# Optimization experiments

Hardware: AMD Instinct MI355X
Metric: run time of the kernel (lower is better)

Reference implementation:

```python
import jax, jax.numpy as jnp
import numpy as np

B, D_IN, H = 8192, 4096, 128
E, N, C = 3, 256, 32          # experts, codebook_size, codebook_dim
D1, D2 = 512, 256             # down_units
U1, U2 = 256, 512             # up_units
CW = 0.25                     # commitment_weight


def setup_inputs() -> dict:
    key = jax.random.key(0)
    ks = jax.random.split(key, 16)
    s = 0.02
    f32 = jnp.float32
    inp = {
        'x':   jax.random.normal(ks[0], (B, D_IN), f32),
        # llm_down MLP: 4096 -> 512 -> 256 -> 128 (ReLU on hiddens, linear out)
        'Wd1': jax.random.normal(ks[1], (D_IN, D1), f32) * s, 'bd1': jnp.zeros((D1,), f32),
        'Wd2': jax.random.normal(ks[2], (D1, D2), f32) * s,  'bd2': jnp.zeros((D2,), f32),
        'Wd3': jax.random.normal(ks[3], (D2, H), f32) * s,   'bd3': jnp.zeros((H,), f32),
        # per-expert VQ: project_in 128->32, codebook [256,32], project_out 32->128
        'Win':  jax.random.normal(ks[4], (E, H, C), f32) * s, 'bin_': jnp.zeros((E, C), f32),
        'codebook': jax.random.normal(ks[5], (E, N, C), f32),
        'Wout': jax.random.normal(ks[6], (E, C, H), f32) * s, 'bout': jnp.zeros((E, H), f32),
        # llm_up MLP: 128 -> 256 -> 512 -> 4096
        'Wu1': jax.random.normal(ks[7], (H, U1), f32) * s,   'bu1': jnp.zeros((U1,), f32),
        'Wu2': jax.random.normal(ks[8], (U1, U2), f32) * s,  'bu2': jnp.zeros((U2,), f32),
        'Wu3': jax.random.normal(ks[9], (U2, D_IN), f32) * s, 'bu3': jnp.zeros((D_IN,), f32),
    }
    return inp


def _decorrelation_loss(qemb):
    # qemb: [B, E, H]
    b, e, h = qemb.shape
    cen = qemb - qemb.mean(axis=0, keepdims=True)
    cen = cen.transpose(1, 0, 2).reshape(e, -1)          # [E, B*H]
    cov = (cen @ cen.T) / (b * h - 1)                    # [E, E]
    std = jnp.sqrt(jnp.diag(cov))
    std = jnp.where(std > 1e-8, std, 1.0)
    corr = cov / jnp.outer(std, std)
    c2 = corr ** 2
    return c2.sum() - jnp.diag(c2).sum()


def _vq_experts(latent, Win, bin_, codebook, Wout, bout):
    # latent: [B,H]; all experts share the same (unmasked) latent.
    xe = jnp.einsum('bh,ehc->ebc', latent, Win) + bin_[:, None, :]      # [E,B,C]
    d2 = ((xe ** 2).sum(-1)[..., None]
          - 2.0 * jnp.einsum('ebc,enc->ebn', xe, codebook)
          + (codebook ** 2).sum(-1)[:, None, :])                        # [E,B,N]
    idx = jnp.argmin(d2, axis=-1)                                       # [E,B]
    q = jax.vmap(lambda c, i: c[i])(codebook, idx)                      # [E,B,C] gather
    commit = CW * jnp.mean((jax.lax.stop_gradient(q) - xe) ** 2, axis=(1, 2)).sum()
    quant = xe + jax.lax.stop_gradient(q - xe)                          # straight-through
    qe = jnp.einsum('ebc,ech->ebh', quant, Wout) + bout[:, None, :]     # [E,B,H]
    return qe, idx, commit


def reference(x, Wd1, bd1, Wd2, bd2, Wd3, bd3, Win, bin_, codebook, Wout, bout,
              Wu1, bu1, Wu2, bu2, Wu3, bu3):
    h = jax.nn.relu(x @ Wd1 + bd1)
    h = jax.nn.relu(h @ Wd2 + bd2)
    latent = h @ Wd3 + bd3                                              # [B,128]
    qe, idx, total_commit = _vq_experts(latent, Win, bin_, codebook, Wout, bout)
    qemb = qe.transpose(1, 0, 2)                                        # [B,E,H]
    decorr = _decorrelation_loss(qemb)
    rl = qemb.mean(axis=1)                                              # [B,H]
    u = jax.nn.relu(rl @ Wu1 + bu1)
    u = jax.nn.relu(u @ Wu2 + bu2)
    recon = jnp.clip(u @ Wu3 + bu3, -1.0, 1.0)                          # [B,4096]
    return (recon, idx.T, total_commit, decorr)
```

## Files before the change

### kernel.cpp

```cpp
#include <hip/hip_runtime.h>
#include <hip/hip_bf16.h>

using bf16 = __hip_bfloat16;

typedef __bf16 bf16x8 __attribute__((ext_vector_type(8)));
typedef float  f32x4  __attribute__((ext_vector_type(4)));
typedef unsigned int u32x4 __attribute__((ext_vector_type(4)));
typedef unsigned long long u64;
typedef unsigned short u16;
typedef unsigned int u32;

__device__ __forceinline__ float b2f(bf16 v) { return __bfloat162float(v); }
__device__ __forceinline__ bf16  f2b(float v) { return __float2bfloat16(v); }
__device__ __forceinline__ u16   bits(bf16 v) { return __builtin_bit_cast(u16, v); }

static constexpr size_t SZ_WD1S = 512ull  * 12288 * 2;
static constexpr size_t SZ_WD2S = 256ull  * 1536  * 2;
static constexpr size_t SZ_WFUS = 128ull  * 768   * 2;
static constexpr size_t SZ_WU1T = 256ull  * 128   * 2;
static constexpr size_t SZ_WU2T = 512ull  * 256   * 2;
static constexpr size_t SZ_WU3T = 4096ull * 512   * 2;
static constexpr size_t SZ_H1S  = 8192ull * 1536  * 2;
static constexpr size_t SZ_H2S  = 8192ull * 768   * 2;
static constexpr size_t SZ_XE   = 8192ull * 128   * 4;
static constexpr size_t SZ_QEMB = 3ull * 8192 * 128 * 4;
static constexpr size_t SZ_RL   = 8192ull * 128   * 2;
static constexpr size_t SZ_U1   = 8192ull * 256   * 2;
static constexpr size_t SZ_U2   = 8192ull * 512   * 2;
static constexpr size_t SZ_CNRM = 768ull * 4;
static constexpr size_t SZ_BFUS = 128ull * 4;
static constexpr size_t SZ_PART = 4ull * 8192 * 512 * 4;

static constexpr size_t OFF_WD1S = 0;
static constexpr size_t OFF_WD2S = OFF_WD1S + SZ_WD1S;
static constexpr size_t OFF_WFUS = OFF_WD2S + SZ_WD2S;
static constexpr size_t OFF_WU1T = OFF_WFUS + SZ_WFUS;
static constexpr size_t OFF_WU2T = OFF_WU1T + SZ_WU1T;
static constexpr size_t OFF_WU3T = OFF_WU2T + SZ_WU2T;
static constexpr size_t OFF_H1S  = OFF_WU3T + SZ_WU3T;
static constexpr size_t OFF_H2S  = OFF_H1S  + SZ_H1S;
static constexpr size_t OFF_XE   = OFF_H2S  + SZ_H2S;
static constexpr size_t OFF_QEMB = OFF_XE   + SZ_XE;
static constexpr size_t OFF_RL   = OFF_QEMB + SZ_QEMB;
static constexpr size_t OFF_U1   = OFF_RL   + SZ_RL;
static constexpr size_t OFF_U2   = OFF_U1   + SZ_U1;
static constexpr size_t OFF_CNRM = OFF_U2   + SZ_U2;
static constexpr size_t OFF_BFUS = OFF_CNRM + ((SZ_CNRM + 255) & ~size_t(255));
static constexpr size_t OFF_STAT = OFF_BFUS + ((SZ_BFUS + 255) & ~size_t(255));
static constexpr size_t OFF_PART = OFF_STAT + 2048;

__global__ void wtrans_bf16(const float* __restrict__ in, bf16* __restrict__ out,
                            int K, int N)
{
    __shared__ float tile[32][33];
    const int tx = threadIdx.x, ty = threadIdx.y;
    const int n0 = blockIdx.x * 32, k0 = blockIdx.y * 32;
    #pragma unroll
    for (int i = 0; i < 32; i += 8)
        tile[ty + i][tx] = in[(size_t)(k0 + ty + i) * N + n0 + tx];
    __syncthreads();
    #pragma unroll
    for (int i = 0; i < 32; i += 8)
        out[(size_t)(n0 + ty + i) * K + k0 + tx] = f2b(tile[tx][ty + i]);
}

__global__ void wtrans_split3(const float* __restrict__ in, bf16* __restrict__ out,
                              int K, int N)
{
    __shared__ float tile[32][33];
    const int tx = threadIdx.x, ty = threadIdx.y;
    const int n0 = blockIdx.x * 32, k0 = blockIdx.y * 32;
    #pragma unroll
    for (int i = 0; i < 32; i += 8)
        tile[ty + i][tx] = in[(size_t)(k0 + ty + i) * N + n0 + tx];
    __syncthreads();
    #pragma unroll
    for (int i = 0; i < 32; i += 8) {
        const float v = tile[tx][ty + i];
        const bf16 hi = f2b(v);
        const bf16 lo = f2b(v - b2f(hi));
        bf16* o = out + (size_t)(n0 + ty + i) * 3 * K + 3 * (k0 + tx);
        o[0] = hi; o[1] = lo; o[2] = hi;
    }
}

__global__ void cnorm_kernel(const float* __restrict__ cb, float* __restrict__ cnorm)
{
    const int i = blockIdx.x * blockDim.x + threadIdx.x;
    if (i < 768) {
        float s = 0.f;
        for (int k = 0; k < 32; ++k) { const float v = cb[i * 32 + k]; s += v * v; }
        cnorm[i] = s;
    }
}

__global__ __launch_bounds__(256)
void wfuse_kernel(const float* __restrict__ Wd3, const float* __restrict__ bd3,
                  const float* __restrict__ Win, const float* __restrict__ bin_,
                  bf16* __restrict__ BtS, float* __restrict__ bfuse)
{
    const int n = blockIdx.x;
    const int t = threadIdx.x;
    if (n >= 96) {
        bf16* o = BtS + (size_t)n * 768 + 3 * t;
        o[0] = f2b(0.f); o[1] = f2b(0.f); o[2] = f2b(0.f);
        if (t == 0) bfuse[n] = 0.f;
        return;
    }
    const int e = n >> 5, c = n & 31;
    float s = 0.f;
    for (int h = 0; h < 128; ++h)
        s += Wd3[t * 128 + h] * Win[(size_t)(e * 128 + h) * 32 + c];
    const bf16 hi = f2b(s);
    const bf16 lo = f2b(s - b2f(hi));
    bf16* o = BtS + (size_t)n * 768 + 3 * t;
    o[0] = hi; o[1] = lo; o[2] = hi;
    if (t == 0) {
        float b = bin_[e * 32 + c];
        for (int h = 0; h < 128; ++h)
            b += bd3[h] * Win[(size_t)(e * 128 + h) * 32 + c];
        bfuse[n] = b;
    }
}

__global__ __launch_bounds__(256)
void gemm1_x3(const float* __restrict__ A, const bf16* __restrict__ Bs3,
              float* __restrict__ part)
{
    __shared__ bf16 As[3 * 4096];
    __shared__ bf16 Bs[3 * 4096];
    const int t = threadIdx.x, lane = t & 63, w = t >> 6;
    const int n0 = blockIdx.x * 128;
    const int m0 = blockIdx.y * 128;
    const int kz = blockIdx.z;
    const int wr = w >> 1, wc = w & 1, l15 = lane & 15, quad = lane >> 4;
    const int laneoff = (l15 >> 1) * 64 + (((((l15 & 1) << 2) | quad) ^ ((l15 >> 1) & 7)) << 3);

    f32x4 acc[4][4];
    #pragma unroll
    for (int i = 0; i < 4; ++i)
        #pragma unroll
        for (int j = 0; j < 4; ++j)
            #pragma unroll
            for (int r = 0; r < 4; ++r) acc[i][j][r] = 0.f;

    const int arow = t >> 1, ahalf = t & 1;
    const int ar2 = arow >> 1, arb = (arow & 1) << 2, arx = ar2 & 7;

    int brow[6], bcol[6];
    #pragma unroll
    for (int i = 0; i < 6; ++i) {
        const int p = i * 256 + t;
        const int bkk = p >> 9, br2 = (p >> 3) & 63;
        const int c3 = (p & 7) ^ (br2 & 7);
        brow[i] = 2 * br2 + (c3 >> 2);
        bcol[i] = bkk * 32 + (c3 & 3) * 8;
    }

    const int s0 = kz * 43;
    const int s1 = (kz == 2) ? 128 : (s0 + 43);
    for (int ks = s0; ks < s1; ++ks) {
        const int ko = ks * 32;
        const float* ap = A + (size_t)(m0 + arow) * 4096 + ko + ahalf * 16;
        float f[16];
        *(float4*)(f + 0)  = *(const float4*)(ap + 0);
        *(float4*)(f + 4)  = *(const float4*)(ap + 4);
        *(float4*)(f + 8)  = *(const float4*)(ap + 8);
        *(float4*)(f + 12) = *(const float4*)(ap + 12);
        #pragma unroll
        for (int i = 0; i < 6; ++i) {
            const bf16* gb = Bs3 + (size_t)(n0 + brow[i]) * 12288 + ko * 3 + bcol[i];
            __builtin_amdgcn_global_load_lds(
                (const __attribute__((address_space(1))) void*)gb,
                (__attribute__((address_space(3))) void*)(Bs + (size_t)(i * 256 + t) * 8), 16, 0, 0);
        }
        u32 hi[16], lo[16];
        #pragma unroll
        for (int k = 0; k < 16; ++k) {
            const bf16 hh = f2b(f[k]);
            hi[k] = bits(hh);
            lo[k] = bits(f2b(f[k] - b2f(hh)));
        }
        #pragma unroll
        for (int j = 0; j < 6; ++j) {
            const int cir = ahalf * 6 + j;
            const int kk = cir >> 2, q = cir & 3;
            u32x4 wv;
            #pragma unroll
            for (int i2 = 0; i2 < 4; ++i2) {
                const int e0 = j * 8 + i2 * 2, e1 = e0 + 1;
                const u32 a0 = ((e0 % 3) < 2) ? hi[e0 / 3] : lo[e0 / 3];
                const u32 a1 = ((e1 % 3) < 2) ? hi[e1 / 3] : lo[e1 / 3];
                wv[i2] = a0 | (a1 << 16);
            }
            *(u32x4*)(As + kk * 4096 + ar2 * 64 + (((arb | q) ^ arx) << 3)) = wv;
        }
        __syncthreads();
        #pragma unroll
        for (int kk = 0; kk < 3; ++kk) {
            bf16x8 af[4], bfr[4];
            #pragma unroll
            for (int mi = 0; mi < 4; ++mi)
                af[mi] = *(const bf16x8*)(As + kk * 4096 + wr * 2048 + mi * 512 + laneoff);
            #pragma unroll
            for (int ni = 0; ni < 4; ++ni)
                bfr[ni] = *(const bf16x8*)(Bs + kk * 4096 + wc * 2048 + ni * 512 + laneoff);
            #pragma unroll
            for (int mi = 0; mi < 4; ++mi)
                #pragma unroll
                for (int ni = 0; ni < 4; ++ni)
                    acc[mi][ni] = __builtin_amdgcn_mfma_f32_16x16x32_bf16(
                        af[mi], bfr[ni], acc[mi][ni], 0, 0, 0);
        }
        __syncthreads();
    }

    float* op = part + (size_t)kz * (8192ull * 512);
    #pragma unroll
    for (int mi = 0; mi < 4; ++mi)
        #pragma unroll
        for (int ni = 0; ni < 4; ++ni) {
            const int col = n0 + wc * 64 + ni * 16 + l15;
            #pragma unroll
            for (int r = 0; r < 4; ++r) {
                const int row = m0 + wr * 64 + mi * 16 + quad * 4 + r;
                op[(size_t)row * 512 + col] = acc[mi][ni][r];
            }
        }
}

__global__ __launch_bounds__(256)
void h1_epi(const float* __restrict__ part, const float* __restrict__ bias,
            bf16* __restrict__ out)
{
    const int idx = blockIdx.x * 256 + threadIdx.x;
    const int r = idx >> 7, c4 = idx & 127;
    const size_t base = (size_t)r * 512 + c4 * 4;
    const float4 p0 = *(const float4*)(part + 0ull * 8192 * 512 + base);
    const float4 p1 = *(const float4*)(part + 1ull * 8192 * 512 + base);
    const float4 p2 = *(const float4*)(part + 2ull * 8192 * 512 + base);
    const float4 bv = *(const float4*)(bias + c4 * 4);
    float v[4];
    v[0] = p0.x + p1.x + p2.x + bv.x;
    v[1] = p0.y + p1.y + p2.y + bv.y;
    v[2] = p0.z + p1.z + p2.z + bv.z;
    v[3] = p0.w + p1.w + p2.w + bv.w;
    u64 h[4], l[4];
    #pragma unroll
    for (int j = 0; j < 4; ++j) {
        const float vv = v[j] > 0.f ? v[j] : 0.f;
        const bf16 hi = f2b(vv);
        h[j] = bits(hi);
        l[j] = bits(f2b(vv - b2f(hi)));
    }
    const u64 w0 = h[0] | (h[0] << 16) | (l[0] << 32) | (h[1] << 48);
    const u64 w1 = h[1] | (l[1] << 16) | (h[2] << 32) | (h[2] << 48);
    const u64 w2 = l[2] | (h[3] << 16) | (h[3] << 32) | (l[3] << 48);
    u64* dst = (u64*)(out + (size_t)r * 1536 + 12 * c4);
    dst[0] = w0; dst[1] = w1; dst[2] = w2;
}

template <int EPI, int RELU>
__global__ __launch_bounds__(256)
void gemm_bt(const bf16* __restrict__ A, const bf16* __restrict__ Bt,
             const float* __restrict__ bias, void* __restrict__ outp,
             int M, int N, int K)
{
    __shared__ bf16 As[128 * 64];
    __shared__ bf16 Bs[128 * 64];
    const int t = threadIdx.x, lane = t & 63, w = t >> 6;
    const int n0 = blockIdx.x * 128;
    const int m0 = blockIdx.y * 128;
    const int wr = w >> 1, wc = w & 1, l15 = lane & 15, quad = lane >> 4;
    const int l7 = l15 & 7;

    f32x4 acc[4][4];
    #pragma unroll
    for (int i = 0; i < 4; ++i)
        #pragma unroll
        for (int j = 0; j < 4; ++j)
            #pragma unroll
            for (int r = 0; r < 4; ++r) acc[i][j][r] = 0.f;

    int lrow[4], lcol[4];
    #pragma unroll
    for (int i = 0; i < 4; ++i) {
        const int c = i * 256 + t;
        lrow[i] = c >> 3;
        lcol[i] = ((c & 7) ^ (lrow[i] & 7)) * 8;
    }

    for (int k0 = 0; k0 < K; k0 += 64) {
        #pragma unroll
        for (int i = 0; i < 4; ++i) {
            const int c = i * 256 + t;
            const bf16* ga = A  + (size_t)(m0 + lrow[i]) * K + k0 + lcol[i];
            const bf16* gb = Bt + (size_t)(n0 + lrow[i]) * K + k0 + lcol[i];
            __builtin_amdgcn_global_load_lds(
                (const __attribute__((address_space(1))) void*)ga,
                (__attribute__((address_space(3))) void*)(As + (size_t)c * 8), 16, 0, 0);
            __builtin_amdgcn_global_load_lds(
                (const __attribute__((address_space(1))) void*)gb,
                (__attribute__((address_space(3))) void*)(Bs + (size_t)c * 8), 16, 0, 0);
        }
        __syncthreads();
        #pragma unroll
        for (int kk = 0; kk < 2; ++kk) {
            const int sw = (((kk << 2) | quad) ^ l7) << 3;
            bf16x8 af[4], bfr[4];
            #pragma unroll
            for (int mi = 0; mi < 4; ++mi)
                af[mi] = *(const bf16x8*)(As + (wr * 64 + mi * 16 + l15) * 64 + sw);
            #pragma unroll
            for (int ni = 0; ni < 4; ++ni)
                bfr[ni] = *(const bf16x8*)(Bs + (wc * 64 + ni * 16 + l15) * 64 + sw);
            #pragma unroll
            for (int mi = 0; mi < 4; ++mi)
                #pragma unroll
                for (int ni = 0; ni < 4; ++ni)
                    acc[mi][ni] = __builtin_amdgcn_mfma_f32_16x16x32_bf16(
                        af[mi], bfr[ni], acc[mi][ni], 0, 0, 0);
        }
        __syncthreads();
    }

    #pragma unroll
    for (int mi = 0; mi < 4; ++mi)
        #pragma unroll
        for (int ni = 0; ni < 4; ++ni) {
            const int col = n0 + wc * 64 + ni * 16 + l15;
            const float bv = bias[col];
            #pragma unroll
            for (int r = 0; r < 4; ++r) {
                const int row = m0 + wr * 64 + mi * 16 + quad * 4 + r;
                float v = acc[mi][ni][r] + bv;
                if (RELU) v = v > 0.f ? v : 0.f;
                if (EPI == 0) {
                    ((float*)outp)[(size_t)row * N + col] = v;
                } else if (EPI == 1) {
                    const bf16 hi = f2b(v);
                    const bf16 lo = f2b(v - b2f(hi));
                    bf16* o = (bf16*)outp + (size_t)row * 3 * N + 3 * col;
                    o[0] = hi; o[1] = hi; o[2] = lo;
                } else if (EPI == 2) {
                    ((bf16*)outp)[(size_t)row * N + col] = f2b(v);
                } else {
                    v = fminf(fmaxf(v, -1.f), 1.f);
                    ((float*)outp)[(size_t)row * N + col] = v;
                }
            }
        }
}

__global__ __launch_bounds__(256)
void vq2_kernel(const float* __restrict__ xe_buf, const float* __restrict__ cb,
                const float* __restrict__ cnorm, const float* __restrict__ Wout,
                const float* __restrict__ bout, float* __restrict__ qemb,
                float* __restrict__ idx_out, float* __restrict__ commit_acc)
{
    __shared__ float cb_s[256 * 36];
    __shared__ float wo_s[32 * 128];
    __shared__ float cn_s[256];
    __shared__ float bo_s[128];
    __shared__ float xe_s[4 * 32];
    __shared__ float q_s[4 * 32];
    __shared__ int   idx_s[4];
    __shared__ u64   wred[4][4];
    __shared__ float cred[256];

    const int e  = blockIdx.x >> 6;
    const int rb = blockIdx.x & 63;
    const int t = threadIdx.x, lane = t & 63, w = t >> 6;

    for (int j = t; j < 256 * 32; j += 256) {
        const int code = j >> 5, c = j & 31;
        cb_s[code * 36 + c] = cb[(size_t)e * 8192 + j];
    }
    for (int j = t; j < 4096; j += 256) wo_s[j] = Wout[(size_t)e * 4096 + j];
    cn_s[t] = cnorm[e * 256 + t];
    if (t < 128) bo_s[t] = bout[e * 128 + t];
    float commit_loc = 0.f;
    __syncthreads();

    for (int it = 0; it < 32; ++it) {
        const int r0 = rb * 128 + it * 4;
        if (t < 128) {
            const int r4 = t >> 5, c = t & 31;
            xe_s[r4 * 32 + c] = xe_buf[(size_t)(r0 + r4) * 128 + e * 32 + c];
        }
        __syncthreads();

        u64 key[4];
        {
            const float4* cp = (const float4*)(cb_s + t * 36);
            const float cn = cn_s[t];
            #pragma unroll
            for (int r4 = 0; r4 < 4; ++r4) {
                float dot = 0.f;
                #pragma unroll
                for (int c4 = 0; c4 < 8; ++c4) {
                    const float4 cv = cp[c4];
                    const float4 xv = *(const float4*)(xe_s + r4 * 32 + c4 * 4);
                    dot += xv.x * cv.x + xv.y * cv.y + xv.z * cv.z + xv.w * cv.w;
                }
                const float d = cn - 2.f * dot;
                u32 ub = __builtin_bit_cast(u32, d);
                ub = (ub & 0x80000000u) ? ~ub : (ub | 0x80000000u);
                key[r4] = ((u64)ub << 32) | (u32)t;
            }
        }
        #pragma unroll
        for (int off = 32; off; off >>= 1) {
            #pragma unroll
            for (int r4 = 0; r4 < 4; ++r4) {
                const u64 o = __shfl_down(key[r4], off, 64);
                if (o < key[r4]) key[r4] = o;
            }
        }
        if (lane == 0) {
            #pragma unroll
            for (int r4 = 0; r4 < 4; ++r4) wred[r4][w] = key[r4];
        }
        __syncthreads();
        if (t < 4) {
            u64 k = wred[t][0];
            #pragma unroll
            for (int ww = 1; ww < 4; ++ww) if (wred[t][ww] < k) k = wred[t][ww];
            const int code = (int)(k & 0xFFFFFFFFu);
            idx_s[t] = code;
            idx_out[(size_t)(r0 + t) * 3 + e] = (float)code;
        }
        __syncthreads();
        if (t < 128) {
            const int r4 = t >> 5, c = t & 31;
            const float q = cb_s[idx_s[r4] * 36 + c];
            q_s[r4 * 32 + c] = q;
            const float dd = q - xe_s[r4 * 32 + c];
            commit_loc += dd * dd;
        }
        __syncthreads();
        #pragma unroll
        for (int p = 0; p < 2; ++p) {
            const int j = p * 256 + t;
            const int r4 = j >> 7, h = j & 127;
            float s = bo_s[h];
            #pragma unroll
            for (int c = 0; c < 32; ++c) s += q_s[r4 * 32 + c] * wo_s[c * 128 + h];
            qemb[((size_t)e * 8192 + r0 + r4) * 128 + h] = s;
        }
        __syncthreads();
    }

    cred[t] = commit_loc;
    __syncthreads();
    for (int o = 128; o; o >>= 1) { if (t < o) cred[t] += cred[t + o]; __syncthreads(); }
    if (t == 0) atomicAdd(commit_acc, cred[0]);
}

__global__ __launch_bounds__(256)
void rlmean_kernel(const float* __restrict__ qemb, bf16* __restrict__ rl,
                   float* __restrict__ meanAcc)
{
    const int t = threadIdx.x, h = t & 127, half = t >> 7;
    const int r0 = blockIdx.x * 64;
    float a0 = 0.f, a1 = 0.f, a2 = 0.f;
    for (int r = r0 + half; r < r0 + 64; r += 2) {
        const float v0 = qemb[((size_t)0 * 8192 + r) * 128 + h];
        const float v1 = qemb[((size_t)1 * 8192 + r) * 128 + h];
        const float v2 = qemb[((size_t)2 * 8192 + r) * 128 + h];
        a0 += v0; a1 += v1; a2 += v2;
        rl[(size_t)r * 128 + h] = f2b((v0 + v1 + v2) * (1.f / 3.f));
    }
    __shared__ float red[3][256];
    red[0][t] = a0; red[1][t] = a1; red[2][t] = a2;
    __syncthreads();
    if (t < 128) {
        atomicAdd(&meanAcc[0 * 128 + h], red[0][t] + red[0][t + 128]);
        atomicAdd(&meanAcc[1 * 128 + h], red[1][t] + red[1][t + 128]);
        atomicAdd(&meanAcc[2 * 128 + h], red[2][t] + red[2][t + 128]);
    }
}

__global__ __launch_bounds__(256)
void gram_kernel(const float* __restrict__ qemb, const float* __restrict__ meanAcc,
                 double* __restrict__ gram)
{
    const int t = threadIdx.x;
    const int h = t & 127, half = t >> 7;
    const int b0 = blockIdx.x * 32;
    const float m0 = meanAcc[0 * 128 + h] * (1.f / 8192.f);
    const float m1 = meanAcc[1 * 128 + h] * (1.f / 8192.f);
    const float m2 = meanAcc[2 * 128 + h] * (1.f / 8192.f);
    float g[6] = {0, 0, 0, 0, 0, 0};
    for (int b = b0 + half; b < b0 + 32; b += 2) {
        const float v0 = qemb[((size_t)0 * 8192 + b) * 128 + h] - m0;
        const float v1 = qemb[((size_t)1 * 8192 + b) * 128 + h] - m1;
        const float v2 = qemb[((size_t)2 * 8192 + b) * 128 + h] - m2;
        g[0] += v0 * v0; g[1] += v0 * v1; g[2] += v0 * v2;
        g[3] += v1 * v1; g[4] += v1 * v2; g[5] += v2 * v2;
    }
    __shared__ float red[256];
    for (int i = 0; i < 6; ++i) {
        red[t] = g[i];
        __syncthreads();
        for (int o = 128; o; o >>= 1) { if (t < o) red[t] += red[t + o]; __syncthreads(); }
        if (t == 0) atomicAdd(&gram[i], (double)red[0]);
        __syncthreads();
    }
}

__global__ void final_kernel(const float* __restrict__ commit_acc,
                             const double* __restrict__ gram,
                             float* __restrict__ out2)
{
    if (threadIdx.x != 0 || blockIdx.x != 0) return;
    const double denom = 8192.0 * 128.0 - 1.0;
    const double c00 = gram[0] / denom, c01 = gram[1] / denom, c02 = gram[2] / denom;
    const double c11 = gram[3] / denom, c12 = gram[4] / denom, c22 = gram[5] / denom;
    double s0 = sqrt(c00), s1 = sqrt(c11), s2 = sqrt(c22);
    if (!(s0 > 1e-8)) s0 = 1.0;
    if (!(s1 > 1e-8)) s1 = 1.0;
    if (!(s2 > 1e-8)) s2 = 1.0;
    const double r01 = c01 / (s0 * s1), r02 = c02 / (s0 * s2), r12 = c12 / (s1 * s2);
    const double decorr = 2.0 * (r01 * r01 + r02 * r02 + r12 * r12);
    out2[0] = (float)((double)commit_acc[0] * (0.25 / (8192.0 * 32.0)));
    out2[1] = (float)decorr;
}

extern "C" void kernel_launch(void* const* d_in, const int* in_sizes, int n_in,
                              void* d_out, int out_size, void* d_ws, size_t ws_size,
                              hipStream_t stream)
{
    const float* x    = (const float*)d_in[0];
    const float* Wd1  = (const float*)d_in[1];
    const float* bd1  = (const float*)d_in[2];
    const float* Wd2  = (const float*)d_in[3];
    const float* bd2  = (const float*)d_in[4];
    const float* Wd3  = (const float*)d_in[5];
    const float* bd3  = (const float*)d_in[6];
    const float* Win  = (const float*)d_in[7];
    const float* bin_ = (const float*)d_in[8];
    const float* cb   = (const float*)d_in[9];
    const float* Wout = (const float*)d_in[10];
    const float* bout = (const float*)d_in[11];
    const float* Wu1  = (const float*)d_in[12];
    const float* bu1  = (const float*)d_in[13];
    const float* Wu2  = (const float*)d_in[14];
    const float* bu2  = (const float*)d_in[15];
    const float* Wu3  = (const float*)d_in[16];
    const float* bu3  = (const float*)d_in[17];

    char* ws = (char*)d_ws;
    bf16*  Wd1s   = (bf16*)(ws + OFF_WD1S);
    bf16*  Wd2s   = (bf16*)(ws + OFF_WD2S);
    bf16*  WfuseS = (bf16*)(ws + OFF_WFUS);
    bf16*  Wu1T   = (bf16*)(ws + OFF_WU1T);
    bf16*  Wu2T   = (bf16*)(ws + OFF_WU2T);
    bf16*  Wu3T   = (bf16*)(ws + OFF_WU3T);
    bf16*  h1s    = (bf16*)(ws + OFF_H1S);
    bf16*  h2s    = (bf16*)(ws + OFF_H2S);
    float* xe     = (float*)(ws + OFF_XE);
    float* qemb   = (float*)(ws + OFF_QEMB);
    bf16*  rl     = (bf16*)(ws + OFF_RL);
    bf16*  u1     = (bf16*)(ws + OFF_U1);
    bf16*  u2     = (bf16*)(ws + OFF_U2);
    float* cnorm  = (float*)(ws + OFF_CNRM);
    float* bfuse  = (float*)(ws + OFF_BFUS);
    float* commit = (float*)(ws + OFF_STAT);
    double* gram  = (double*)(ws + OFF_STAT + 8);
    float* meanA  = (float*)(ws + OFF_STAT + 64);
    float* part   = (float*)(ws + OFF_PART);

    float* out_f   = (float*)d_out;
    float* idx_out = out_f + (size_t)8192 * 4096;
    float* scal    = idx_out + (size_t)8192 * 3;

    hipMemsetAsync(ws + OFF_STAT, 0, 2048, stream);

    const dim3 tb(32, 8);
    wtrans_split3<<<dim3(16, 128), tb, 0, stream>>>(Wd1, Wd1s, 4096, 512);
    wtrans_split3<<<dim3(8, 16),   tb, 0, stream>>>(Wd2, Wd2s, 512, 256);
    wtrans_bf16<<<dim3(8, 4),      tb, 0, stream>>>(Wu1, Wu1T, 128, 256);
    wtrans_bf16<<<dim3(16, 8),     tb, 0, stream>>>(Wu2, Wu2T, 256, 512);
    wtrans_bf16<<<dim3(128, 16),   tb, 0, stream>>>(Wu3, Wu3T, 512, 4096);
    cnorm_kernel<<<3, 256, 0, stream>>>(cb, cnorm);
    wfuse_kernel<<<128, 256, 0, stream>>>(Wd3, bd3, Win, bin_, WfuseS, bfuse);

    gemm1_x3<<<dim3(4, 64, 3), 256, 0, stream>>>(x, Wd1s, part);
    h1_epi<<<4096, 256, 0, stream>>>(part, bd1, h1s);
    gemm_bt<1, 1><<<dim3(2, 64), 256, 0, stream>>>(h1s, Wd2s, bd2, h2s, 8192, 256, 1536);
    gemm_bt<0, 0><<<dim3(1, 64), 256, 0, stream>>>(h2s, WfuseS, bfuse, xe, 8192, 128, 768);

    vq2_kernel<<<192, 256, 0, stream>>>(xe, cb, cnorm, Wout, bout, qemb, idx_out, commit);
    rlmean_kernel<<<128, 256, 0, stream>>>(qemb, rl, meanA);
    gram_kernel<<<256, 256, 0, stream>>>(qemb, meanA, gram);
    final_kernel<<<1, 64, 0, stream>>>(commit, gram, scal);

    gemm_bt<2, 1><<<dim3(2, 64),  256, 0, stream>>>(rl, Wu1T, bu1, u1,    8192, 256,  128);
    gemm_bt<2, 1><<<dim3(4, 64),  256, 0, stream>>>(u1, Wu2T, bu2, u2,    8192, 512,  256);
    gemm_bt<3, 0><<<dim3(32, 64), 256, 0, stream>>>(u2, Wu3T, bu3, out_f, 8192, 4096, 512);

    (void)in_sizes; (void)n_in; (void)out_size; (void)ws_size;
}
```

Before: 704.8 us.

## Store Wd1 as separate hi/lo bf16 halves and use split-K of four in gemm1

Wd1 is no longer stored as an interleaved 3x-expanded hi/lo/hi matrix. It is now laid out as [hi(32) | lo(32)] per 32-wide K chunk, which shrinks the B footprint from 3x to 2x. gemm1 now issues three MFMAs per hi/lo pair (hh, lh, hl) from separate operand fragments, with simpler swizzled LDS tiles of 128x64. This cuts B-side global traffic and shared-memory size. The split-K factor goes from 3 to 4 with even 32-step ranges, and launch_bounds asks for 4 blocks per CU to raise occupancy. The cost is one more partial buffer that the epilogue must read.

```diff
diff --git a/kernel.cpp b/kernel.cpp
--- a/kernel.cpp
+++ b/kernel.cpp
@@ -14,7 +14,7 @@
 __device__ __forceinline__ bf16  f2b(float v) { return __float2bfloat16(v); }
 __device__ __forceinline__ u16   bits(bf16 v) { return __builtin_bit_cast(u16, v); }
 
-static constexpr size_t SZ_WD1S = 512ull  * 12288 * 2;
+static constexpr size_t SZ_WD1S = 512ull  * 8192  * 2;
 static constexpr size_t SZ_WD2S = 256ull  * 1536  * 2;
 static constexpr size_t SZ_WFUS = 128ull  * 768   * 2;
 static constexpr size_t SZ_WU1T = 256ull  * 128   * 2;
@@ -84,6 +84,27 @@
     }
 }
 
+__global__ void wtrans_hilo(const float* __restrict__ in, bf16* __restrict__ out,
+                            int K, int N)
+{
+    __shared__ float tile[32][33];
+    const int tx = threadIdx.x, ty = threadIdx.y;
+    const int n0 = blockIdx.x * 32, k0 = blockIdx.y * 32;
+    #pragma unroll
+    for (int i = 0; i < 32; i += 8)
+        tile[ty + i][tx] = in[(size_t)(k0 + ty + i) * N + n0 + tx];
+    __syncthreads();
+    const int kg = k0 >> 5;
+    #pragma unroll
+    for (int i = 0; i < 32; i += 8) {
+        const float v = tile[tx][ty + i];
+        const bf16 hi = f2b(v);
+        const bf16 lo = f2b(v - b2f(hi));
+        bf16* o = out + (size_t)(n0 + ty + i) * 8192 + kg * 64 + tx;
+        o[0] = hi; o[32] = lo;
+    }
+}
+
 __global__ void cnorm_kernel(const float* __restrict__ cb, float* __restrict__ cnorm)
 {
     const int i = blockIdx.x * blockDim.x + threadIdx.x;
@@ -123,18 +144,19 @@
     }
 }
 
-__global__ __launch_bounds__(256)
-void gemm1_x3(const float* __restrict__ A, const bf16* __restrict__ Bs3,
+__global__ __launch_bounds__(256, 4)
+void gemm1_x3(const float* __restrict__ A, const bf16* __restrict__ Bhl,
               float* __restrict__ part)
 {
-    __shared__ bf16 As[3 * 4096];
-    __shared__ bf16 Bs[3 * 4096];
+    __shared__ bf16 As[128 * 64];
+    __shared__ bf16 Bs[128 * 64];
     const int t = threadIdx.x, lane = t & 63, w = t >> 6;
     const int n0 = blockIdx.x * 128;
     const int m0 = blockIdx.y * 128;
     const int kz = blockIdx.z;
     const int wr = w >> 1, wc = w & 1, l15 = lane & 15, quad = lane >> 4;
-    const int laneoff = (l15 >> 1) * 64 + (((((l15 & 1) << 2) | quad) ^ ((l15 >> 1) & 7)) << 3);
+    const int offh = ((quad ^ (l15 & 7)) << 3);
+    const int offl = offh ^ 32;
 
     f32x4 acc[4][4];
     #pragma unroll
@@ -144,73 +166,77 @@
             #pragma unroll
             for (int r = 0; r < 4; ++r) acc[i][j][r] = 0.f;
 
-    const int arow = t >> 1, ahalf = t & 1;
-    const int ar2 = arow >> 1, arb = (arow & 1) << 2, arx = ar2 & 7;
-
-    int brow[6], bcol[6];
-    #pragma unroll
-    for (int i = 0; i < 6; ++i) {
+    const int arow = t >> 1, ahalf = t & 1, arx = arow & 7;
+    bf16* const aw0 = As + arow * 64 + (((ahalf * 2 + 0) ^ arx) << 3);
+    bf16* const aw1 = As + arow * 64 + (((ahalf * 2 + 1) ^ arx) << 3);
+    bf16* const aw2 = As + arow * 64 + (((4 + ahalf * 2 + 0) ^ arx) << 3);
+    bf16* const aw3 = As + arow * 64 + (((4 + ahalf * 2 + 1) ^ arx) << 3);
+
+    int brow[4], bco[4];
+    #pragma unroll
+    for (int i = 0; i < 4; ++i) {
         const int p = i * 256 + t;
-        const int bkk = p >> 9, br2 = (p >> 3) & 63;
-        const int c3 = (p & 7) ^ (br2 & 7);
-        brow[i] = 2 * br2 + (c3 >> 2);
-        bcol[i] = bkk * 32 + (c3 & 3) * 8;
-    }
-
-    const int s0 = kz * 43;
-    const int s1 = (kz == 2) ? 128 : (s0 + 43);
+        brow[i] = p >> 3;
+        bco[i] = ((p & 7) ^ (brow[i] & 7)) * 8;
+    }
+
+    const int s0 = kz * 32, s1 = s0 + 32;
     for (int ks = s0; ks < s1; ++ks) {
-        const int ko = ks * 32;
-        const float* ap = A + (size_t)(m0 + arow) * 4096 + ko + ahalf * 16;
+        const float* ap = A + (size_t)(m0 + arow) * 4096 + ks * 32 + ahalf * 16;
         float f[16];
         *(float4*)(f + 0)  = *(const float4*)(ap + 0);
         *(float4*)(f + 4)  = *(const float4*)(ap + 4);
         *(float4*)(f + 8)  = *(const float4*)(ap + 8);
         *(float4*)(f + 12) = *(const float4*)(ap + 12);
         #pragma unroll
-        for (int i = 0; i < 6; ++i) {
-            const bf16* gb = Bs3 + (size_t)(n0 + brow[i]) * 12288 + ko * 3 + bcol[i];
+        for (int i = 0; i < 4; ++i) {
+            const bf16* gb = Bhl + (size_t)(n0 + brow[i]) * 8192 + ks * 64 + bco[i];
             __builtin_amdgcn_global_load_lds(
                 (const __attribute__((address_space(1))) void*)gb,
                 (__attribute__((address_space(3))) void*)(Bs + (size_t)(i * 256 + t) * 8), 16, 0, 0);
         }
-        u32 hi[16], lo[16];
-        #pragma unroll
-        for (int k = 0; k < 16; ++k) {
-            const bf16 hh = f2b(f[k]);
-            hi[k] = bits(hh);
-            lo[k] = bits(f2b(f[k] - b2f(hh)));
-        }
-        #pragma unroll
-        for (int j = 0; j < 6; ++j) {
-            const int cir = ahalf * 6 + j;
-            const int kk = cir >> 2, q = cir & 3;
-            u32x4 wv;
-            #pragma unroll
-            for (int i2 = 0; i2 < 4; ++i2) {
-                const int e0 = j * 8 + i2 * 2, e1 = e0 + 1;
-                const u32 a0 = ((e0 % 3) < 2) ? hi[e0 / 3] : lo[e0 / 3];
-                const u32 a1 = ((e1 % 3) < 2) ? hi[e1 / 3] : lo[e1 / 3];
-                wv[i2] = a0 | (a1 << 16);
-            }
-            *(u32x4*)(As + kk * 4096 + ar2 * 64 + (((arb | q) ^ arx) << 3)) = wv;
-        }
-        __syncthreads();
-        #pragma unroll
-        for (int kk = 0; kk < 3; ++kk) {
-            bf16x8 af[4], bfr[4];
-            #pragma unroll
-            for (int mi = 0; mi < 4; ++mi)
-                af[mi] = *(const bf16x8*)(As + kk * 4096 + wr * 2048 + mi * 512 + laneoff);
-            #pragma unroll
-            for (int ni = 0; ni < 4; ++ni)
-                bfr[ni] = *(const bf16x8*)(Bs + kk * 4096 + wc * 2048 + ni * 512 + laneoff);
-            #pragma unroll
-            for (int mi = 0; mi < 4; ++mi)
+        {
+            u32x4 hv, lv;
+            #pragma unroll
+            for (int j = 0; j < 4; ++j) {
+                const bf16 h0 = f2b(f[2 * j]), h1 = f2b(f[2 * j + 1]);
+                const u32 l0 = bits(f2b(f[2 * j] - b2f(h0)));
+                const u32 l1 = bits(f2b(f[2 * j + 1] - b2f(h1)));
+                hv[j] = (u32)bits(h0) | ((u32)bits(h1) << 16);
+                lv[j] = l0 | (l1 << 16);
+            }
+            *(u32x4*)aw0 = hv; *(u32x4*)aw2 = lv;
+            #pragma unroll
+            for (int j = 0; j < 4; ++j) {
+                const bf16 h0 = f2b(f[8 + 2 * j]), h1 = f2b(f[8 + 2 * j + 1]);
+                const u32 l0 = bits(f2b(f[8 + 2 * j] - b2f(h0)));
+                const u32 l1 = bits(f2b(f[8 + 2 * j + 1] - b2f(h1)));
+                hv[j] = (u32)bits(h0) | ((u32)bits(h1) << 16);
+                lv[j] = l0 | (l1 << 16);
+            }
+            *(u32x4*)aw1 = hv; *(u32x4*)aw3 = lv;
+        }
+        __syncthreads();
+        {
+            bf16x8 ah[4], al[4];
+            #pragma unroll
+            for (int mi = 0; mi < 4; ++mi) {
+                const bf16* ar = As + (wr * 64 + mi * 16 + l15) * 64;
+                ah[mi] = *(const bf16x8*)(ar + offh);
+                al[mi] = *(const bf16x8*)(ar + offl);
+            }
+            #pragma unroll
+            for (int ni = 0; ni < 4; ++ni) {
+                const bf16* br = Bs + (wc * 64 + ni * 16 + l15) * 64;
+                const bf16x8 bh = *(const bf16x8*)(br + offh);
+                const bf16x8 bl = *(const bf16x8*)(br + offl);
                 #pragma unroll
-                for (int ni = 0; ni < 4; ++ni)
-                    acc[mi][ni] = __builtin_amdgcn_mfma_f32_16x16x32_bf16(
-                        af[mi], bfr[ni], acc[mi][ni], 0, 0, 0);
+                for (int mi = 0; mi < 4; ++mi) {
+                    acc[mi][ni] = __builtin_amdgcn_mfma_f32_16x16x32_bf16(ah[mi], bh, acc[mi][ni], 0, 0, 0);
+                    acc[mi][ni] = __builtin_amdgcn_mfma_f32_16x16x32_bf16(al[mi], bh, acc[mi][ni], 0, 0, 0);
+                    acc[mi][ni] = __builtin_amdgcn_mfma_f32_16x16x32_bf16(ah[mi], bl, acc[mi][ni], 0, 0, 0);
+                }
+            }
         }
         __syncthreads();
     }
@@ -239,12 +265,13 @@
     const float4 p0 = *(const float4*)(part + 0ull * 8192 * 512 + base);
     const float4 p1 = *(const float4*)(part + 1ull * 8192 * 512 + base);
     const float4 p2 = *(const float4*)(part + 2ull * 8192 * 512 + base);
+    const float4 p3 = *(const float4*)(part + 3ull * 8192 * 512 + base);
     const float4 bv = *(const float4*)(bias + c4 * 4);
     float v[4];
-    v[0] = p0.x + p1.x + p2.x + bv.x;
-    v[1] = p0.y + p1.y + p2.y + bv.y;
-    v[2] = p0.z + p1.z + p2.z + bv.z;
-    v[3] = p0.w + p1.w + p2.w + bv.w;
+    v[0] = p0.x + p1.x + p2.x + p3.x + bv.x;
+    v[1] = p0.y + p1.y + p2.y + p3.y + bv.y;
+    v[2] = p0.z + p1.z + p2.z + p3.z + bv.z;
+    v[3] = p0.w + p1.w + p2.w + p3.w + bv.w;
     u64 h[4], l[4];
     #pragma unroll
     for (int j = 0; j < 4; ++j) {
@@ -578,7 +605,7 @@
     hipMemsetAsync(ws + OFF_STAT, 0, 2048, stream);
 
     const dim3 tb(32, 8);
-    wtrans_split3<<<dim3(16, 128), tb, 0, stream>>>(Wd1, Wd1s, 4096, 512);
+    wtrans_hilo<<<dim3(16, 128), tb, 0, stream>>>(Wd1, Wd1s, 4096, 512);
     wtrans_split3<<<dim3(8, 16),   tb, 0, stream>>>(Wd2, Wd2s, 512, 256);
     wtrans_bf16<<<dim3(8, 4),      tb, 0, stream>>>(Wu1, Wu1T, 128, 256);
     wtrans_bf16<<<dim3(16, 8),     tb, 0, stream>>>(Wu2, Wu2T, 256, 512);
@@ -586,7 +613,7 @@
     cnorm_kernel<<<3, 256, 0, stream>>>(cb, cnorm);
     wfuse_kernel<<<128, 256, 0, stream>>>(Wd3, bd3, Win, bin_, WfuseS, bfuse);
 
-    gemm1_x3<<<dim3(4, 64, 3), 256, 0, stream>>>(x, Wd1s, part);
+    gemm1_x3<<<dim3(4, 64, 4), 256, 0, stream>>>(x, Wd1s, part);
     h1_epi<<<4096, 256, 0, stream>>>(part, bd1, h1s);
     gemm_bt<1, 1><<<dim3(2, 64), 256, 0, stream>>>(h1s, Wd2s, bd2, h2s, 8192, 256, 1536);
     gemm_bt<0, 0><<<dim3(1, 64), 256, 0, stream>>>(h2s, WfuseS, bfuse, xe, 8192, 128, 768);
```

Result: faster. 627.0 us (-11.0%).
